# Optimization experiments

Measured on AMD Instinct MI355X. Metric: run time of the kernel, lower is better.

The kernel has to match this reference:

```python
import math
import jax, jax.numpy as jnp
import numpy as np

B, L, N, D = 256, 50, 100000, 128

def _make_pe(max_len, d_model):
    # matches torch PositionalEncoding buffer (sin/cos scaled by 1/1000)
    pe = np.zeros((max_len, d_model), dtype=np.float32)
    position = np.arange(max_len, dtype=np.float32)[:, None]
    div_term = np.exp(np.arange(0, d_model, 2, dtype=np.float32) * (-math.log(10000.0) / d_model))
    pe[:, 0::2] = np.sin(position * div_term) / 1000.0
    pe[:, 1::2] = np.cos(position * div_term) / 1000.0
    return jnp.asarray(pe)

def setup_inputs() -> dict:
    key = jax.random.key(0)
    ks = jax.random.split(key, 8)
    g = 1.414  # xavier gain used in the torch module
    seeds = jax.random.randint(ks[0], (B, L), 0, N)
    labels = jax.random.randint(ks[1], (B,), 0, N)
    E = jax.random.normal(ks[2], (N, D), dtype=jnp.float32) * 0.02
    W1 = jax.random.normal(ks[3], (D, D), dtype=jnp.float32) * (g * math.sqrt(2.0 / (D + D)))
    W2 = jax.random.normal(ks[4], (D, D), dtype=jnp.float32) * (g * math.sqrt(2.0 / (D + D)))
    q = jax.random.normal(ks[5], (D,), dtype=jnp.float32) * (g * math.sqrt(2.0 / (1 + D)))
    b_att = jax.random.normal(ks[6], (1,), dtype=jnp.float32) * 0.01
    out_bias = jax.random.normal(ks[7], (N,), dtype=jnp.float32) * 0.01
    pe = _make_pe(L, D)
    return {"seeds": seeds, "labels": labels, "E": E, "W1": W1, "W2": W2,
            "q": q, "b_att": b_att, "out_bias": out_bias, "pe": pe}

def reference(seeds, labels, E, W1, W2, q, b_att, out_bias, pe):
    # user_representation: gather seed embeddings, add positional encoding (eval mode: dropout is identity)
    v = E[seeds] + pe[None, :, :]                 # (B, L, D)
    vn = v[:, -1, :]                              # (B, D) last element of each seed set
    # SoftAttention: att_i = q @ (W1 @ v_i + W2 @ vn + b); no softmax in original
    inp = jnp.einsum('bld,ed->ble', v, W1) + jnp.einsum('bd,ed->be', vn, W2)[:, None, :] + b_att[0]
    att = jnp.einsum('ble,e->bl', inp, q)         # (B, L) raw attention weights
    u = jnp.einsum('bl,bld->bd', att, v)          # (B, D) user representations
    # scores = F.linear(u, E, out_bias)
    scores = u @ E.T + out_bias                   # (B, N)
    logp = jax.nn.log_softmax(scores, axis=-1)
    base_loss = -jnp.mean(jnp.take_along_axis(logp, labels[:, None], axis=1))
    return scores, base_loss
```

## Files before the change

kernel.cpp:

```cpp
#include <hip/hip_runtime.h>
#include <hip/hip_bf16.h>

#define B_SZ 256
#define L_SZ 50
#define N_SZ 100000
#define D_SZ 128
#define NB ((N_SZ + 127) / 128)

typedef __attribute__((ext_vector_type(8))) short bf16x8;
typedef __attribute__((ext_vector_type(4))) float f32x4;

__device__ inline unsigned short f2bf(float f) {
    union { float f; unsigned u; } v; v.f = f;
    unsigned r = v.u + 0x7FFFu + ((v.u >> 16) & 1u);
    return (unsigned short)(r >> 16);
}

__global__ __launch_bounds__(128) void k_prep(const float* __restrict__ W1,
                                              const float* __restrict__ W2,
                                              const float* __restrict__ q,
                                              float* __restrict__ wsf,
                                              float* __restrict__ loss_slot) {
    int d = threadIdx.x;
    float a1 = 0.f, a2 = 0.f;
    #pragma unroll 4
    for (int e = 0; e < D_SZ; ++e) {
        float qe = q[e];
        a1 += qe * W1[e * D_SZ + d];
        a2 += qe * W2[e * D_SZ + d];
    }
    wsf[d] = a1;
    wsf[D_SZ + d] = a2;
    __shared__ float red[D_SZ];
    red[d] = q[d];
    __syncthreads();
    if (d == 0) {
        float s = 0.f;
        for (int i = 0; i < D_SZ; ++i) s += red[i];
        wsf[2 * D_SZ] = s;
        loss_slot[0] = 0.f;
    }
}

__global__ __launch_bounds__(128) void k_ub(const int* __restrict__ seeds,
                                            const float* __restrict__ E,
                                            const float* __restrict__ pe,
                                            const float* __restrict__ wsf,
                                            const float* __restrict__ b_att,
                                            unsigned short* __restrict__ u_bf) {
    __shared__ float vbuf[L_SZ][D_SZ + 1];
    __shared__ float att[L_SZ];
    __shared__ float c2s;
    __shared__ float qw1s[D_SZ], qw2s[D_SZ];
    int b = blockIdx.x, d = threadIdx.x;
    qw1s[d] = wsf[d];
    qw2s[d] = wsf[D_SZ + d];

    for (int l = 0; l < L_SZ; ++l) {
        int s = seeds[b * L_SZ + l];
        vbuf[l][d] = E[(size_t)s * D_SZ + d] + pe[l * D_SZ + d];
    }
    __syncthreads();

    if (d < L_SZ) {
        float acc = 0.f;
        #pragma unroll 4
        for (int k = 0; k < D_SZ; ++k) acc += vbuf[d][k] * qw1s[k];
        att[d] = acc;
    } else if (d == L_SZ) {
        float acc = 0.f;
        #pragma unroll 4
        for (int k = 0; k < D_SZ; ++k) acc += vbuf[L_SZ - 1][k] * qw2s[k];
        c2s = acc;
    }
    __syncthreads();

    float add = c2s + b_att[0] * wsf[2 * D_SZ];
    float u = 0.f;
    #pragma unroll 5
    for (int l = 0; l < L_SZ; ++l) u += (att[l] + add) * vbuf[l][d];
    u_bf[b * D_SZ + d] = f2bf(u);
}

__global__ __launch_bounds__(512, 4) void k_gemm(const float* __restrict__ E,
                                                 const float* __restrict__ out_bias,
                                                 const unsigned short* __restrict__ u_bf,
                                                 float* __restrict__ scores,
                                                 float* __restrict__ partial) {
    __shared__ unsigned short us[B_SZ * D_SZ];
    __shared__ float lds_sum[B_SZ];
    int tid = threadIdx.x;
    int w = tid >> 6, lane = tid & 63;
    if (tid < B_SZ) lds_sum[tid] = 0.f;

    #pragma unroll
    for (int r = 0; r < 8; ++r) {
        int d = r * 8192 + tid * 16;
        int b = d >> 8, inrow = d & 255;
        bf16x8 v = *(const bf16x8*)((const char*)u_bf + d);
        *(bf16x8*)((char*)us + b * 256 + (inrow ^ ((b & 7) << 4))) = v;
    }

    int nc = blockIdx.x * 128 + w * 16;
    bool valid = (nc < N_SZ);
    int lo = lane & 15, hi = lane >> 4;
    int kb = hi * 8;

    long erow = valid ? (nc + lo) : 0;
    bf16x8 efrag[4];
    #pragma unroll
    for (int ks = 0; ks < 4; ++ks) {
        const float* p = E + (size_t)erow * D_SZ + ks * 32 + kb;
        float4 x = *(const float4*)p;
        float4 y = *(const float4*)(p + 4);
        bf16x8 f;
        f[0] = (short)f2bf(x.x); f[1] = (short)f2bf(x.y);
        f[2] = (short)f2bf(x.z); f[3] = (short)f2bf(x.w);
        f[4] = (short)f2bf(y.x); f[5] = (short)f2bf(y.y);
        f[6] = (short)f2bf(y.z); f[7] = (short)f2bf(y.w);
        efrag[ks] = f;
    }
    int nb = valid ? (nc + hi * 4) : 0;
    float4 bias4 = *(const float4*)(out_bias + nb);

    __syncthreads();

    f32x4 acc[16];
    #pragma unroll
    for (int i = 0; i < 16; ++i) acc[i] = (f32x4){0.f, 0.f, 0.f, 0.f};

    #pragma unroll
    for (int ks = 0; ks < 4; ++ks) {
        int kcol = ks * 64 + hi * 16;
        #pragma unroll
        for (int rs = 0; rs < 16; ++rs) {
            int b = rs * 16 + lo;
            bf16x8 uf = *(const bf16x8*)((const char*)us + b * 256 + (kcol ^ ((b & 7) << 4)));
            acc[rs] = __builtin_amdgcn_mfma_f32_16x16x32_bf16(efrag[ks], uf, acc[rs], 0, 0, 0);
        }
    }

    #pragma unroll
    for (int rs = 0; rs < 16; ++rs) {
        int jr = rs * 16 + lo;
        f32x4 c;
        c[0] = acc[rs][0] + bias4.x;
        c[1] = acc[rs][1] + bias4.y;
        c[2] = acc[rs][2] + bias4.z;
        c[3] = acc[rs][3] + bias4.w;
        if (valid)
            *(f32x4*)(scores + (size_t)jr * N_SZ + nb) = c;
        float p = __expf(c[0]) + __expf(c[1]) + __expf(c[2]) + __expf(c[3]);
        p += __shfl_xor(p, 16);
        p += __shfl_xor(p, 32);
        if (valid && hi == 0) atomicAdd(&lds_sum[jr], p);
    }
    __syncthreads();
    if (tid < B_SZ) partial[(size_t)blockIdx.x * B_SZ + tid] = lds_sum[tid];
}

__global__ __launch_bounds__(256) void k_loss(const float* __restrict__ partial,
                                              const float* __restrict__ scores,
                                              const int* __restrict__ labels,
                                              float* __restrict__ out_loss) {
    int b = blockIdx.x, t = threadIdx.x;
    float acc = 0.f;
    for (int i = t; i < NB; i += 256) acc += partial[(size_t)i * B_SZ + b];
    __shared__ float red[256];
    red[t] = acc;
    __syncthreads();
    for (int s = 128; s > 0; s >>= 1) {
        if (t < s) red[t] += red[t + s];
        __syncthreads();
    }
    if (t == 0) {
        int lab = labels[b];
        float val = scores[(size_t)b * N_SZ + lab] - logf(red[0]);
        atomicAdd(out_loss, -val * (1.0f / (float)B_SZ));
    }
}

extern "C" void kernel_launch(void* const* d_in, const int* in_sizes, int n_in,
                              void* d_out, int out_size, void* d_ws, size_t ws_size,
                              hipStream_t stream) {
    const int*   seeds    = (const int*)d_in[0];
    const int*   labels   = (const int*)d_in[1];
    const float* E        = (const float*)d_in[2];
    const float* W1       = (const float*)d_in[3];
    const float* W2       = (const float*)d_in[4];
    const float* q        = (const float*)d_in[5];
    const float* b_att    = (const float*)d_in[6];
    const float* out_bias = (const float*)d_in[7];
    const float* pe       = (const float*)d_in[8];

    float* scores = (float*)d_out;
    float* loss   = scores + (size_t)B_SZ * N_SZ;

    float*          wsf     = (float*)d_ws;
    unsigned short* u_bf    = (unsigned short*)((char*)d_ws + 2048);
    float*          partial = (float*)((char*)d_ws + 67584);

    k_prep<<<1, 128, 0, stream>>>(W1, W2, q, wsf, loss);
    k_ub<<<B_SZ, 128, 0, stream>>>(seeds, E, pe, wsf, b_att, u_bf);
    k_gemm<<<NB, 512, 0, stream>>>(E, out_bias, u_bf, scores, partial);
    k_loss<<<B_SZ, 256, 0, stream>>>(partial, scores, labels, loss);
}
```

Baseline: 62.88 us.

## Fold prep into user-rep kernel and split GEMM into smaller half-batch blocks

```diff
diff --git a/kernel.cpp b/kernel.cpp
--- a/kernel.cpp
+++ b/kernel.cpp
@@ -5,7 +5,7 @@
 #define L_SZ 50
 #define N_SZ 100000
 #define D_SZ 128
-#define NB ((N_SZ + 127) / 128)
+#define NBT ((N_SZ + 63) / 64)
 
 typedef __attribute__((ext_vector_type(8))) short bf16x8;
 typedef __attribute__((ext_vector_type(4))) float f32x4;
@@ -16,50 +16,37 @@
     return (unsigned short)(r >> 16);
 }
 
-__global__ __launch_bounds__(128) void k_prep(const float* __restrict__ W1,
-                                              const float* __restrict__ W2,
-                                              const float* __restrict__ q,
-                                              float* __restrict__ wsf,
-                                              float* __restrict__ loss_slot) {
-    int d = threadIdx.x;
-    float a1 = 0.f, a2 = 0.f;
-    #pragma unroll 4
-    for (int e = 0; e < D_SZ; ++e) {
-        float qe = q[e];
-        a1 += qe * W1[e * D_SZ + d];
-        a2 += qe * W2[e * D_SZ + d];
-    }
-    wsf[d] = a1;
-    wsf[D_SZ + d] = a2;
-    __shared__ float red[D_SZ];
-    red[d] = q[d];
-    __syncthreads();
-    if (d == 0) {
-        float s = 0.f;
-        for (int i = 0; i < D_SZ; ++i) s += red[i];
-        wsf[2 * D_SZ] = s;
-        loss_slot[0] = 0.f;
-    }
-}
-
 __global__ __launch_bounds__(128) void k_ub(const int* __restrict__ seeds,
                                             const float* __restrict__ E,
                                             const float* __restrict__ pe,
-                                            const float* __restrict__ wsf,
+                                            const float* __restrict__ W1,
+                                            const float* __restrict__ W2,
+                                            const float* __restrict__ q,
                                             const float* __restrict__ b_att,
-                                            unsigned short* __restrict__ u_bf) {
+                                            unsigned short* __restrict__ u_bf,
+                                            float* __restrict__ loss_slot) {
     __shared__ float vbuf[L_SZ][D_SZ + 1];
     __shared__ float att[L_SZ];
-    __shared__ float c2s;
-    __shared__ float qw1s[D_SZ], qw2s[D_SZ];
+    __shared__ float qs[D_SZ], qw1s[D_SZ], qw2s[D_SZ];
+    __shared__ float c2s, qsums;
     int b = blockIdx.x, d = threadIdx.x;
-    qw1s[d] = wsf[d];
-    qw2s[d] = wsf[D_SZ + d];
+    qs[d] = q[d];
 
     for (int l = 0; l < L_SZ; ++l) {
         int s = seeds[b * L_SZ + l];
         vbuf[l][d] = E[(size_t)s * D_SZ + d] + pe[l * D_SZ + d];
     }
+    __syncthreads();
+
+    float a1 = 0.f, a2 = 0.f;
+    #pragma unroll 4
+    for (int e = 0; e < D_SZ; ++e) {
+        float qe = qs[e];
+        a1 += qe * W1[e * D_SZ + d];
+        a2 += qe * W2[e * D_SZ + d];
+    }
+    qw1s[d] = a1;
+    qw2s[d] = a2;
     __syncthreads();
 
     if (d < L_SZ) {
@@ -72,36 +59,44 @@
         #pragma unroll 4
         for (int k = 0; k < D_SZ; ++k) acc += vbuf[L_SZ - 1][k] * qw2s[k];
         c2s = acc;
+    } else if (d == L_SZ + 1) {
+        float s = 0.f;
+        for (int i = 0; i < D_SZ; ++i) s += qs[i];
+        qsums = s;
     }
     __syncthreads();
 
-    float add = c2s + b_att[0] * wsf[2 * D_SZ];
+    float add = c2s + b_att[0] * qsums;
     float u = 0.f;
     #pragma unroll 5
     for (int l = 0; l < L_SZ; ++l) u += (att[l] + add) * vbuf[l][d];
     u_bf[b * D_SZ + d] = f2bf(u);
+
+    if (b == 0 && d == 0) loss_slot[0] = 0.f;
 }
 
-__global__ __launch_bounds__(512, 4) void k_gemm(const float* __restrict__ E,
+__global__ __launch_bounds__(256, 4) void k_gemm(const float* __restrict__ E,
                                                  const float* __restrict__ out_bias,
                                                  const unsigned short* __restrict__ u_bf,
                                                  float* __restrict__ scores,
                                                  float* __restrict__ partial) {
-    __shared__ unsigned short us[B_SZ * D_SZ];
-    __shared__ float lds_sum[B_SZ];
+    __shared__ unsigned short us[128 * D_SZ];
+    __shared__ float lds_sum[128];
     int tid = threadIdx.x;
     int w = tid >> 6, lane = tid & 63;
-    if (tid < B_SZ) lds_sum[tid] = 0.f;
+    int tile = blockIdx.x >> 1, hf = blockIdx.x & 1;
+    if (tid < 128) lds_sum[tid] = 0.f;
 
+    const char* ub = (const char*)u_bf + hf * 32768;
     #pragma unroll
     for (int r = 0; r < 8; ++r) {
-        int d = r * 8192 + tid * 16;
-        int b = d >> 8, inrow = d & 255;
-        bf16x8 v = *(const bf16x8*)((const char*)u_bf + d);
+        int off = r * 4096 + tid * 16;
+        int b = off >> 8, inrow = off & 255;
+        bf16x8 v = *(const bf16x8*)(ub + off);
         *(bf16x8*)((char*)us + b * 256 + (inrow ^ ((b & 7) << 4))) = v;
     }
 
-    int nc = blockIdx.x * 128 + w * 16;
+    int nc = tile * 64 + w * 16;
     bool valid = (nc < N_SZ);
     int lo = lane & 15, hi = lane >> 4;
     int kb = hi * 8;
@@ -125,38 +120,32 @@
 
     __syncthreads();
 
-    f32x4 acc[16];
     #pragma unroll
-    for (int i = 0; i < 16; ++i) acc[i] = (f32x4){0.f, 0.f, 0.f, 0.f};
-
-    #pragma unroll
-    for (int ks = 0; ks < 4; ++ks) {
-        int kcol = ks * 64 + hi * 16;
+    for (int rs = 0; rs < 8; ++rs) {
+        f32x4 acc = (f32x4){0.f, 0.f, 0.f, 0.f};
         #pragma unroll
-        for (int rs = 0; rs < 16; ++rs) {
+        for (int ks = 0; ks < 4; ++ks) {
             int b = rs * 16 + lo;
+            int kcol = ks * 64 + hi * 16;
             bf16x8 uf = *(const bf16x8*)((const char*)us + b * 256 + (kcol ^ ((b & 7) << 4)));
-            acc[rs] = __builtin_amdgcn_mfma_f32_16x16x32_bf16(efrag[ks], uf, acc[rs], 0, 0, 0);
+            acc = __builtin_amdgcn_mfma_f32_16x16x32_bf16(efrag[ks], uf, acc, 0, 0, 0);
         }
-    }
-
-    #pragma unroll
-    for (int rs = 0; rs < 16; ++rs) {
-        int jr = rs * 16 + lo;
+        int jl = rs * 16 + lo;
+        int jr = hf * 128 + jl;
         f32x4 c;
-        c[0] = acc[rs][0] + bias4.x;
-        c[1] = acc[rs][1] + bias4.y;
-        c[2] = acc[rs][2] + bias4.z;
-        c[3] = acc[rs][3] + bias4.w;
+        c[0] = acc[0] + bias4.x;
+        c[1] = acc[1] + bias4.y;
+        c[2] = acc[2] + bias4.z;
+        c[3] = acc[3] + bias4.w;
         if (valid)
             *(f32x4*)(scores + (size_t)jr * N_SZ + nb) = c;
         float p = __expf(c[0]) + __expf(c[1]) + __expf(c[2]) + __expf(c[3]);
         p += __shfl_xor(p, 16);
         p += __shfl_xor(p, 32);
-        if (valid && hi == 0) atomicAdd(&lds_sum[jr], p);
+        if (valid && hi == 0) atomicAdd(&lds_sum[jl], p);
     }
     __syncthreads();
-    if (tid < B_SZ) partial[(size_t)blockIdx.x * B_SZ + tid] = lds_sum[tid];
+    if (tid < 128) partial[(size_t)tile * B_SZ + hf * 128 + tid] = lds_sum[tid];
 }
 
 __global__ __launch_bounds__(256) void k_loss(const float* __restrict__ partial,
@@ -165,7 +154,7 @@
                                               float* __restrict__ out_loss) {
     int b = blockIdx.x, t = threadIdx.x;
     float acc = 0.f;
-    for (int i = t; i < NB; i += 256) acc += partial[(size_t)i * B_SZ + b];
+    for (int i = t; i < NBT; i += 256) acc += partial[(size_t)i * B_SZ + b];
     __shared__ float red[256];
     red[t] = acc;
     __syncthreads();
@@ -196,12 +185,10 @@
     float* scores = (float*)d_out;
     float* loss   = scores + (size_t)B_SZ * N_SZ;
 
-    float*          wsf     = (float*)d_ws;
     unsigned short* u_bf    = (unsigned short*)((char*)d_ws + 2048);
     float*          partial = (float*)((char*)d_ws + 67584);
 
-    k_prep<<<1, 128, 0, stream>>>(W1, W2, q, wsf, loss);
-    k_ub<<<B_SZ, 128, 0, stream>>>(seeds, E, pe, wsf, b_att, u_bf);
-    k_gemm<<<NB, 512, 0, stream>>>(E, out_bias, u_bf, scores, partial);
+    k_ub<<<B_SZ, 128, 0, stream>>>(seeds, E, pe, W1, W2, q, b_att, u_bf, loss);
+    k_gemm<<<NBT * 2, 256, 0, stream>>>(E, out_bias, u_bf, scores, partial);
     k_loss<<<B_SZ, 256, 0, stream>>>(partial, scores, labels, loss);
 }
```

Result: slower. 64.82 us (+3.1%).
